# Performance work log

Hardware: AMD Instinct MI355X
Metric: run time of the kernel (lower is better)

The kernel has to match this reference:

```python
import jax, jax.numpy as jnp
import numpy as np
import math


def setup_inputs() -> dict:
    B, L, D, P, V = 4, 4096, 512, 128, 8
    key = jax.random.key(0)
    ki = iter(jax.random.split(key, 40))
    def rn(shape, s=0.02):
        return jax.random.normal(next(ki), shape, jnp.float32) * s
    z = lambda *s: jnp.zeros(s, jnp.float32)
    return dict(
        x=jax.random.normal(next(ki), (B, L, D), jnp.float32),
        W_omega=rn((D, D)), b_omega=z(D),
        omega_scale=jnp.full((D,), 0.01, jnp.float32),
        W_pi1=rn((D, D)), b_pi1=z(D), W_pi2=rn((D, D)), b_pi2=z(D),
        W_m1v=rn((D, D)), b_m1v=z(D),
        W_m1o=rn((D, D)), b_m1o=z(D),
        W_mag=rn((D, D)), b_mag=z(D),
        mag_scale=jnp.asarray(5.0, jnp.float32),
        W_qoff=rn((D, D)), b_qoff=z(D),
        W_kenc=rn((D, P)), b_kenc=z(P),
        W_venc=rn((D, V)), b_venc=z(V),
        W_sk1=rn((2 * D, D)), b_sk1=z(D),
        W_sk2=rn((D, P)), b_sk2=z(P),
        W_sg=rn((D, 1)), b_sg=z(1),
        W_kvo=rn((V, D)), b_kvo=z(D),
        ln_g=jnp.ones((4 * D,), jnp.float32), ln_b=z(4 * D),
        W_o1=rn((4 * D, 2 * D)), b_o1=z(2 * D),
        W_o2=rn((2 * D, D)), b_o2=z(D),
    )


def _lin(h, W, b):
    return h @ W + b


def _gelu(h):
    return jax.nn.gelu(h, approximate=False)  # torch nn.GELU default (erf)


def _forward(x, W_omega, b_omega, omega_scale, W_pi1, b_pi1, W_pi2, b_pi2,
             W_m1v, b_m1v, W_m1o, b_m1o, W_mag, b_mag, mag_scale,
             W_qoff, b_qoff, W_kenc, b_kenc, W_venc, b_venc,
             W_sk1, b_sk1, W_sk2, b_sk2, W_sg, b_sg, W_kvo, b_kvo,
             ln_g, ln_b, W_o1, b_o1, W_o2, b_o2):
    B, L, D = x.shape
    P = W_kenc.shape[1]
    # --- evolving phases ---
    omega_scaled = _lin(x, W_omega, b_omega) * jnp.abs(omega_scale)
    phi_init = _lin(_gelu(_lin(x, W_pi1, b_pi1)), W_pi2, b_pi2)
    phi = phi_init + jnp.cumsum(omega_scaled, axis=1)
    cos_phi, sin_phi = jnp.cos(phi), jnp.sin(phi)
    # --- memory 1: positional phasor memory ---
    v1 = _lin(x, W_m1v, b_m1v)
    magnitude = jax.nn.sigmoid(_lin(x, W_mag, b_mag)) * jnp.abs(mag_scale)
    wv1 = magnitude * v1
    sqrt_mag = jnp.sqrt(jnp.cumsum(magnitude, axis=1) + 1e-8)
    mem1_cos = jnp.cumsum(wv1 * cos_phi, axis=1) / sqrt_mag
    mem1_sin = jnp.cumsum(wv1 * sin_phi, axis=1) / sqrt_mag
    phi_q = phi + _lin(x, W_qoff, b_qoff)
    pos_ret = (mem1_cos * jnp.cos(phi_q) + mem1_sin * jnp.sin(phi_q)) / math.sqrt(D)
    pos_out = _lin(pos_ret, W_m1o, b_m1o)
    # --- memory 2: key/value phasor binding ---
    query_phase = jnp.tanh(_lin(x, W_kenc, b_kenc)) * math.pi
    values = _lin(x, W_venc, b_venc)                      # [B,L,V]
    store_gate = jax.nn.sigmoid(_lin(x, W_sg, b_sg))      # [B,L,1]
    positions = jnp.arange(1, L + 1, dtype=x.dtype)[None, :, None]
    context_avg = jnp.cumsum(x, axis=1) / positions
    sk_in = jnp.concatenate([x, context_avg], axis=-1)
    storage_phase = jnp.tanh(_lin(_gelu(_lin(sk_in, W_sk1, b_sk1)), W_sk2, b_sk2)) * math.pi
    store_cos, store_sin = jnp.cos(storage_phase), jnp.sin(storage_phase)  # [B,L,P]
    gv = values * store_gate                               # [B,L,V]
    # [B,L,P,V] outer products, cumsum along L
    kv_mem_cos = jnp.cumsum(store_cos[..., None] * gv[:, :, None, :], axis=1)
    kv_mem_sin = jnp.cumsum(store_sin[..., None] * gv[:, :, None, :], axis=1)
    gate_cum = jnp.clip(jnp.cumsum(store_gate, axis=1), 1.0, None)  # [B,L,1]
    inv_norm = (1.0 / jnp.sqrt(gate_cum))[..., None]
    kv_mem_cos = kv_mem_cos * inv_norm
    kv_mem_sin = kv_mem_sin * inv_norm
    q_cos, q_sin = jnp.cos(query_phase), jnp.sin(query_phase)
    kv_retrieved = (jnp.einsum('blp,blpv->blv', q_cos, kv_mem_cos)
                    + jnp.einsum('blp,blpv->blv', q_sin, kv_mem_sin)) / math.sqrt(P)
    kv_out = _lin(kv_retrieved, W_kvo, b_kvo)
    # --- output projection ---
    combined = jnp.concatenate([pos_out, kv_out, x * cos_phi, x * sin_phi], axis=-1)
    mu = combined.mean(axis=-1, keepdims=True)
    var = combined.var(axis=-1, keepdims=True)
    h = (combined - mu) / jnp.sqrt(var + 1e-5) * ln_g + ln_b
    h = _gelu(_lin(h, W_o1, b_o1))  # dropout is identity in eval mode
    return x + _lin(h, W_o2, b_o2)


def reference(x, W_omega, b_omega, omega_scale, W_pi1, b_pi1, W_pi2, b_pi2,
              W_m1v, b_m1v, W_m1o, b_m1o, W_mag, b_mag, mag_scale,
              W_qoff, b_qoff, W_kenc, b_kenc, W_venc, b_venc,
              W_sk1, b_sk1, W_sk2, b_sk2, W_sg, b_sg, W_kvo, b_kvo,
              ln_g, ln_b, W_o1, b_o1, W_o2, b_o2):
    return _forward(x, W_omega, b_omega, omega_scale, W_pi1, b_pi1, W_pi2, b_pi2,
                    W_m1v, b_m1v, W_m1o, b_m1o, W_mag, b_mag, mag_scale,
                    W_qoff, b_qoff, W_kenc, b_kenc, W_venc, b_venc,
                    W_sk1, b_sk1, W_sk2, b_sk2, W_sg, b_sg, W_kvo, b_kvo,
                    ln_g, ln_b, W_o1, b_o1, W_o2, b_o2)
```

## Files before the change

### kernel.cpp

```cpp
#include <hip/hip_runtime.h>
#include <math.h>

#define B_ 4
#define L_ 4096
#define D_ 512
#define P_ 128
#define V_ 8
#define N_ (B_*L_)
#define NC 64
#define CL (L_/NC)
#define LD ((size_t)L_*D_)
#define PI_F 3.14159265358979323846f

typedef unsigned short ushort;
typedef __attribute__((ext_vector_type(8))) short bh8;
typedef __attribute__((ext_vector_type(4))) float f4;
typedef const __attribute__((address_space(1))) unsigned int gu32;
typedef __attribute__((address_space(3))) unsigned int lu32;

__device__ __forceinline__ float geluf(float v){
    return 0.5f*v*(1.0f+erff(v*0.7071067811865475f));
}
__device__ __forceinline__ float tanhf_fast(float x){
    return 1.0f - 2.0f/(__expf(2.0f*x)+1.0f);
}
__device__ __forceinline__ ushort f2b(float f){
    union { float f; unsigned u; } v; v.f = f;
    unsigned r = (v.u + 0x7fffu + ((v.u >> 16) & 1u)) >> 16;
    return (ushort)r;
}
__device__ __forceinline__ float b2f(ushort h){
    union { unsigned u; float f; } v; v.u = ((unsigned)h) << 16;
    return v.f;
}
__device__ __forceinline__ void gload16(const ushort* g, ushort* l){
    __builtin_amdgcn_global_load_lds((gu32*)g, (lu32*)l, 16, 0, 0);
}
__device__ __forceinline__ int xcd_swz(int orig, int nwg){
    int q8 = nwg >> 3, r8 = nwg & 7;
    int xcd = orig & 7, sub = orig >> 3;
    return (xcd < r8 ? xcd*(q8+1) : r8*(q8+1) + (xcd-r8)*q8) + sub;
}

template<int ACT>
__global__ __launch_bounds__(512, 1)
void egemm_k(const ushort* __restrict__ A, int lda,
             const ushort* __restrict__ Wt, const float* __restrict__ bias,
             ushort* __restrict__ Ob, float* __restrict__ Of,
             int ldc, int K, const float* __restrict__ addbuf)
{
    __shared__ ushort lA[2][256*64];
    __shared__ ushort lB[2][256*64];
    const int tid = threadIdx.x, lane = tid & 63, w = tid >> 6;
    const int wr = w >> 2, wc = w & 3;
    const int nbx = gridDim.x;
    const int wg = xcd_swz(blockIdx.y*nbx + blockIdx.x, nbx*gridDim.y);
    const int row0 = (wg / nbx) * 256, col0 = (wg % nbx) * 256;

    f4 zero4 = {0.f,0.f,0.f,0.f};
    f4 acc[8][4];
    #pragma unroll
    for (int i=0;i<8;i++)
        #pragma unroll
        for (int j=0;j<4;j++) acc[i][j] = zero4;

    auto stage = [&](int buf, int kt){
        #pragma unroll
        for (int is=0; is<4; ++is){
            int id = tid + is*512;
            int r = id >> 3, p = id & 7;
            int srcc = (p ^ (r & 7)) * 8;
            gload16(A + (size_t)(row0 + r)*lda + kt + srcc, &lA[buf][r*64 + p*8]);
        }
        #pragma unroll
        for (int is=0; is<4; ++is){
            int id = tid + is*512;
            int r = id >> 3, p = id & 7;
            int srcc = (p ^ (r & 7)) * 8;
            gload16(Wt + (size_t)(col0 + r)*K + kt + srcc, &lB[buf][r*64 + p*8]);
        }
    };

    const int NT = K >> 6;
    stage(0, 0);
    for (int t2 = 0; t2 < NT; ++t2){
        int cur = t2 & 1;
        if (t2 + 1 < NT){
            stage(cur ^ 1, (t2+1) << 6);
            asm volatile("s_waitcnt vmcnt(8)" ::: "memory");
        } else {
            asm volatile("s_waitcnt vmcnt(0)" ::: "memory");
        }
        __builtin_amdgcn_s_barrier();
        __builtin_amdgcn_sched_barrier(0);
        __builtin_amdgcn_s_setprio(1);
        #pragma unroll
        for (int h=0; h<2; ++h){
            bh8 af[8], bf_[4];
            #pragma unroll
            for (int i=0;i<8;i++){
                int row = wr*128 + i*16 + (lane & 15);
                int pc = (h*4 + (lane >> 4)) ^ (row & 7);
                af[i] = *(const bh8*)&lA[cur][row*64 + pc*8];
            }
            #pragma unroll
            for (int j=0;j<4;j++){
                int row = wc*64 + j*16 + (lane & 15);
                int pc = (h*4 + (lane >> 4)) ^ (row & 7);
                bf_[j] = *(const bh8*)&lB[cur][row*64 + pc*8];
            }
            #pragma unroll
            for (int i=0;i<8;i++)
                #pragma unroll
                for (int j=0;j<4;j++)
                    acc[i][j] = __builtin_amdgcn_mfma_f32_16x16x32_bf16(af[i], bf_[j], acc[i][j], 0, 0, 0);
        }
        __builtin_amdgcn_s_setprio(0);
        __builtin_amdgcn_sched_barrier(0);
        __builtin_amdgcn_s_barrier();
    }

    #pragma unroll
    for (int i=0;i<8;i++){
        int rr = row0 + wr*128 + i*16 + ((lane >> 4) << 2);
        #pragma unroll
        for (int j=0;j<4;j++){
            int cc = col0 + wc*64 + j*16 + (lane & 15);
            float bv = bias[cc];
            #pragma unroll
            for (int q=0;q<4;q++){
                int r = rr + q;
                float t = acc[i][j][q] + bv;
                if (ACT==2){
                    if (addbuf) t += addbuf[(size_t)r*512 + cc];
                    Of[(size_t)r*ldc + cc] = t;
                } else {
                    if (ACT==1) t = geluf(t);
                    Ob[(size_t)r*ldc + cc] = f2b(t);
                }
            }
        }
    }
}

__global__ __launch_bounds__(256, 2)
void fgemm_k(const ushort* __restrict__ A, int lda, const ushort* __restrict__ Wt,
             const float* __restrict__ bs0, const float* __restrict__ bs1,
             const float* __restrict__ bs2, const float* __restrict__ bs3,
             const float* __restrict__ bs4, const float* __restrict__ bs5,
             ushort* __restrict__ o0, ushort* __restrict__ o1p, ushort* __restrict__ o2p,
             ushort* __restrict__ o3p, ushort* __restrict__ o4p,
             ushort* __restrict__ Qc, ushort* __restrict__ Qs,
             const float* __restrict__ omsc, const float* __restrict__ magscp, int K)
{
    __shared__ ushort lA[2][128*32];
    __shared__ ushort lB[2][128*32];
    const int tid = threadIdx.x, lane = tid & 63, w = tid >> 6;
    const int wr = w >> 1, wc = w & 1;
    const int nbx = gridDim.x;
    const int wg = xcd_swz(blockIdx.y*nbx + blockIdx.x, nbx*gridDim.y);
    const int row0 = (wg / nbx) * 128, col0 = (wg % nbx) * 128;

    const int srow = w*32 + (lane >> 2);
    const int scol = (lane & 3) * 8;
    const ushort* gA0 = A  + (size_t)(row0 + srow)      * lda + scol;
    const ushort* gA1 = A  + (size_t)(row0 + srow + 16) * lda + scol;
    const ushort* gB0 = Wt + (size_t)(col0 + srow)      * K   + scol;
    const ushort* gB1 = Wt + (size_t)(col0 + srow + 16) * K   + scol;
    const int d0 = srow*32 + scol, d1 = (srow+16)*32 + scol;

    f4 zero4 = {0.f,0.f,0.f,0.f};
    f4 acc[4][4];
    #pragma unroll
    for (int i=0;i<4;i++)
        #pragma unroll
        for (int j=0;j<4;j++) acc[i][j] = zero4;

    const int fr = lane & 15, fq = (lane >> 4) * 8;
    gload16(gA0, &lA[0][d0]); gload16(gA1, &lA[0][d1]);
    gload16(gB0, &lB[0][d0]); gload16(gB1, &lB[0][d1]);
    __syncthreads();
    int cur = 0;
    for (int kt = 0; kt < K; kt += 32) {
        int nxt = cur ^ 1;
        if (kt + 32 < K) {
            gload16(gA0 + kt + 32, &lA[nxt][d0]); gload16(gA1 + kt + 32, &lA[nxt][d1]);
            gload16(gB0 + kt + 32, &lB[nxt][d0]); gload16(gB1 + kt + 32, &lB[nxt][d1]);
        }
        bh8 af[4], bfr[4];
        #pragma unroll
        for (int i=0;i<4;i++){
            af[i]  = *(const bh8*)&lA[cur][(wr*64 + i*16 + fr)*32 + fq];
            bfr[i] = *(const bh8*)&lB[cur][(wc*64 + i*16 + fr)*32 + fq];
        }
        #pragma unroll
        for (int i=0;i<4;i++)
            #pragma unroll
            for (int j=0;j<4;j++)
                acc[i][j] = __builtin_amdgcn_mfma_f32_16x16x32_bf16(af[i], bfr[j], acc[i][j], 0, 0, 0);
        __syncthreads();
        cur = nxt;
    }

    const int seg = col0 >> 9;
    if (seg == 5) {
        #pragma unroll
        for (int i=0;i<4;i++){
            int rr = row0 + wr*64 + i*16 + ((lane >> 4) << 2);
            #pragma unroll
            for (int j=0;j<4;j++){
                int lcc = (col0 - 2560) + wc*64 + j*16 + (lane & 15);
                float bv = bs5[lcc];
                #pragma unroll
                for (int q=0;q<4;q++){
                    int r = rr + q;
                    float ph = tanhf_fast(acc[i][j][q] + bv)*PI_F;
                    Qc[(size_t)r*128 + lcc] = f2b(__cosf(ph));
                    Qs[(size_t)r*128 + lcc] = f2b(__sinf(ph));
                }
            }
        }
        return;
    }
    const float* bias = seg==0?bs0: seg==1?bs1: seg==2?bs2: seg==3?bs3: bs4;
    ushort* dst = seg==0?o0: seg==1?o1p: seg==2?o2p: seg==3?o3p: o4p;
    float msc = fabsf(*magscp);
    #pragma unroll
    for (int i=0;i<4;i++){
        int rr = row0 + wr*64 + i*16 + ((lane >> 4) << 2);
        #pragma unroll
        for (int j=0;j<4;j++){
            int cc = col0 + wc*64 + j*16 + (lane & 15);
            int lcc = cc & 511;
            float bv = bias[lcc];
            float csc = (seg==0) ? fabsf(omsc[lcc]) : 1.0f;
            #pragma unroll
            for (int q=0;q<4;q++){
                int r = rr + q;
                float t = acc[i][j][q] + bv;
                if (seg==1)      t = msc/(1.0f+__expf(-t));
                else if (seg==3) t = geluf(t);
                else             t *= csc;
                dst[(size_t)r*512 + lcc] = f2b(t);
            }
        }
    }
}

__global__ __launch_bounds__(256, 2)
void mgemm_k(const ushort* __restrict__ Apos, const ushort* __restrict__ Ask,
             const ushort* __restrict__ Wm1o, const ushort* __restrict__ Wsk2,
             const float* __restrict__ bm1o, const float* __restrict__ bsk2,
             ushort* __restrict__ planes, ushort* __restrict__ Kc, ushort* __restrict__ Ks)
{
    __shared__ ushort lA[2][128*32];
    __shared__ ushort lB[2][128*32];
    const int tid = threadIdx.x, lane = tid & 63, w = tid >> 6;
    const int wr = w >> 1, wc = w & 1;
    const int nbx = gridDim.x;
    const int wg = xcd_swz(blockIdx.y*nbx + blockIdx.x, nbx*gridDim.y);
    const int row0 = (wg / nbx) * 128, col0 = (wg % nbx) * 128;
    const int seg = col0 >> 9;
    const ushort* A  = seg ? Ask  : Apos;
    const ushort* Wt = seg ? Wsk2 : Wm1o;
    const int wcol0 = seg ? (col0 - 512) : col0;
    const int K = 512;

    const int srow = w*32 + (lane >> 2);
    const int scol = (lane & 3) * 8;
    const ushort* gA0 = A  + (size_t)(row0 + srow)       * 512 + scol;
    const ushort* gA1 = A  + (size_t)(row0 + srow + 16)  * 512 + scol;
    const ushort* gB0 = Wt + (size_t)(wcol0 + srow)      * 512 + scol;
    const ushort* gB1 = Wt + (size_t)(wcol0 + srow + 16) * 512 + scol;
    const int d0 = srow*32 + scol, d1 = (srow+16)*32 + scol;

    f4 zero4 = {0.f,0.f,0.f,0.f};
    f4 acc[4][4];
    #pragma unroll
    for (int i=0;i<4;i++)
        #pragma unroll
        for (int j=0;j<4;j++) acc[i][j] = zero4;

    const int fr = lane & 15, fq = (lane >> 4) * 8;
    gload16(gA0, &lA[0][d0]); gload16(gA1, &lA[0][d1]);
    gload16(gB0, &lB[0][d0]); gload16(gB1, &lB[0][d1]);
    __syncthreads();
    int cur = 0;
    for (int kt = 0; kt < K; kt += 32) {
        int nxt = cur ^ 1;
        if (kt + 32 < K) {
            gload16(gA0 + kt + 32, &lA[nxt][d0]); gload16(gA1 + kt + 32, &lA[nxt][d1]);
            gload16(gB0 + kt + 32, &lB[nxt][d0]); gload16(gB1 + kt + 32, &lB[nxt][d1]);
        }
        bh8 af[4], bfr[4];
        #pragma unroll
        for (int i=0;i<4;i++){
            af[i]  = *(const bh8*)&lA[cur][(wr*64 + i*16 + fr)*32 + fq];
            bfr[i] = *(const bh8*)&lB[cur][(wc*64 + i*16 + fr)*32 + fq];
        }
        #pragma unroll
        for (int i=0;i<4;i++)
            #pragma unroll
            for (int j=0;j<4;j++)
                acc[i][j] = __builtin_amdgcn_mfma_f32_16x16x32_bf16(af[i], bfr[j], acc[i][j], 0, 0, 0);
        __syncthreads();
        cur = nxt;
    }

    #pragma unroll
    for (int i=0;i<4;i++){
        int rr = row0 + wr*64 + i*16 + ((lane >> 4) << 2);
        #pragma unroll
        for (int j=0;j<4;j++){
            int cc = col0 + wc*64 + j*16 + (lane & 15);
            #pragma unroll
            for (int q=0;q<4;q++){
                int r = rr + q;
                if (seg == 0){
                    planes[(size_t)r*2048 + cc] = f2b(acc[i][j][q] + bm1o[cc]);
                } else {
                    int lcc = cc - 512;
                    float ph = tanhf_fast(acc[i][j][q] + bsk2[lcc])*PI_F;
                    Kc[(size_t)r*128 + lcc] = f2b(__cosf(ph));
                    Ks[(size_t)r*128 + lcc] = f2b(__sinf(ph));
                }
            }
        }
    }
}

struct WtArgs {
    const float* src[12];
    ushort* dst[12];
    int K[12], M[12], t0[13];
};
__global__ __launch_bounds__(256)
void wtall_k(WtArgs a)
{
    __shared__ float tile[32][33];
    int bb = blockIdx.x;
    int j = 0;
    while (bb >= a.t0[j+1]) ++j;
    int tt = bb - a.t0[j];
    int K = a.K[j], M = a.M[j];
    int mt = M >> 5;
    int kb = (tt / mt) * 32, mb = (tt % mt) * 32;
    const float* W = a.src[j]; ushort* Wt = a.dst[j];
    int tx = threadIdx.x & 31, ty = threadIdx.x >> 5;
    #pragma unroll
    for (int i = ty; i < 32; i += 8)
        tile[i][tx] = W[(size_t)(kb+i)*M + mb+tx];
    __syncthreads();
    #pragma unroll
    for (int i = ty; i < 32; i += 8)
        Wt[(size_t)(mb+i)*K + kb+tx] = f2b(tile[tx][i]);
}

__global__ __launch_bounds__(256)
void fconv_k(const float* __restrict__ in, ushort* __restrict__ xctx)
{
    size_t i = ((size_t)blockIdx.x*256 + threadIdx.x) * 4;
    size_t row = i >> 9; int d = (int)(i & 511);
    float4 v = *(const float4*)(in + i);
    ushort* o = xctx + row*1024 + d;
    o[0]=f2b(v.x); o[1]=f2b(v.y); o[2]=f2b(v.z); o[3]=f2b(v.w);
}

__global__ __launch_bounds__(256)
void s1a_k(const ushort* __restrict__ omega, const float* __restrict__ xg,
           float* __restrict__ csA, float* __restrict__ csX)
{
    int bid = blockIdx.x;
    int b = bid >> 7; int rem = bid & 127;
    int dg = rem & 1, c = rem >> 1;
    int d = dg*256 + threadIdx.x;
    size_t base = ((size_t)b*L_ + (size_t)c*CL)*D_ + d;
    float sA=0.f, sX=0.f;
    for (int l=0;l<CL;l++){
        sA += b2f(omega[base + (size_t)l*D_]);
        sX += xg[base + (size_t)l*D_];
    }
    size_t ci = ((size_t)b*NC + c)*D_ + d;
    csA[ci]=sA; csX[ci]=sX;
}

__global__ __launch_bounds__(256)
void aux1_k(float* __restrict__ csA, float* __restrict__ csX,
            const float* __restrict__ sgate, float* __restrict__ rinv, int nb2)
{
    __shared__ float wsum[4];
    __shared__ float carry;
    int bb = blockIdx.x, t = threadIdx.x;
    if (bb < nb2){
        int tt = bb*256 + t;
        int b = tt >> 9, d = tt & 511;
        float* bufs[2] = {csA, csX};
        #pragma unroll
        for (int i=0;i<2;i++){
            float* p = bufs[i] + ((size_t)b*NC)*D_ + d;
            float run=0.f;
            for (int c=0;c<NC;c++){
                float v = p[(size_t)c*D_];
                p[(size_t)c*D_] = run;
                run += v;
            }
        }
        return;
    }
    int b = bb - nb2;
    int lane = t & 63, wave = t >> 6;
    if (t == 0) carry = 0.f;
    __syncthreads();
    for (int s = 0; s < L_/256; s++){
        float v = sgate[(size_t)b*L_ + s*256 + t];
        float sc = v;
        #pragma unroll
        for (int off=1; off<64; off<<=1){
            float u = __shfl_up(sc, off, 64);
            if (lane >= off) sc += u;
        }
        if (lane == 63) wsum[wave] = sc;
        __syncthreads();
        float woff = carry;
        for (int w2 = 0; w2 < wave; w2++) woff += wsum[w2];
        float inc = sc + woff;
        rinv[(size_t)b*L_ + s*256 + t] = rsqrtf(fmaxf(inc, 1.0f));
        __syncthreads();
        if (t == 255) carry = inc;
        __syncthreads();
    }
}

__global__ void prefix_k(float* a, float* b2v, float* c3, int nbuf)
{
    int t = blockIdx.x*blockDim.x + threadIdx.x;
    int b = t >> 9, d = t & 511;
    float* bufs[3] = {a,b2v,c3};
    for (int i=0;i<nbuf;i++){
        float* p = bufs[i] + ((size_t)b*NC)*D_ + d;
        float run=0.f;
        for (int c=0;c<NC;c++){
            float v = p[(size_t)c*D_];
            p[(size_t)c*D_] = run;
            run += v;
        }
    }
}

__global__ __launch_bounds__(256)
void s1c_k(const ushort* __restrict__ omega, const float* __restrict__ xg,
           const ushort* __restrict__ phi_init,
           const ushort* __restrict__ magn, const ushort* __restrict__ v1,
           const float* __restrict__ csA, const float* __restrict__ csX,
           ushort* __restrict__ cphi, ushort* __restrict__ sphi, ushort* __restrict__ xctx,
           float* __restrict__ csM, float* __restrict__ csC, float* __restrict__ csS)
{
    int bid = blockIdx.x;
    int b = bid >> 7; int rem = bid & 127;
    int dg = rem & 1, c = rem >> 1;
    int d = dg*256 + threadIdx.x;
    size_t ci = ((size_t)b*NC + c)*D_ + d;
    float phiacc = csA[ci], xacc = csX[ci];
    float sM=0.f,sC=0.f,sS=0.f;
    size_t xrow = (size_t)b*L_ + (size_t)c*CL;
    size_t base = xrow*D_ + d;
    for (int l=0;l<CL;l++){
        size_t idx = base + (size_t)l*D_;
        phiacc += b2f(omega[idx]);
        float ph = b2f(phi_init[idx]) + phiacc;
        float spv = __sinf(ph), cpv = __cosf(ph);
        cphi[idx] = f2b(cpv); sphi[idx] = f2b(spv);
        xacc += xg[idx];
        xctx[(xrow + l)*1024 + 512 + d] = f2b(__fdividef(xacc, (float)(c*CL + l + 1)));
        float m = b2f(magn[idx]); sM += m;
        float wv = m * b2f(v1[idx]);
        sC = fmaf(wv, cpv, sC); sS = fmaf(wv, spv, sS);
    }
    csM[ci]=sM; csC[ci]=sC; csS[ci]=sS;
}

__global__ __launch_bounds__(256)
void s1e_k(const ushort* __restrict__ magn, const ushort* __restrict__ v1,
           const ushort* qoff, const ushort* __restrict__ cphi, const ushort* __restrict__ sphi,
           const float* __restrict__ csM, const float* __restrict__ csC,
           const float* __restrict__ csS, ushort* pos_ret)
{
    int bid = blockIdx.x;
    int b = bid >> 7; int rem = bid & 127;
    int dg = rem & 1, c = rem >> 1;
    int d = dg*256 + threadIdx.x;
    size_t ci = ((size_t)b*NC + c)*D_ + d;
    float mA=csM[ci], cA=csC[ci], sA=csS[ci];
    size_t base = ((size_t)b*L_ + (size_t)c*CL)*D_ + d;
    for (int l=0;l<CL;l++){
        size_t idx = base + (size_t)l*D_;
        float m = b2f(magn[idx]); mA += m;
        float wv = m * b2f(v1[idx]);
        float cp = b2f(cphi[idx]), sp = b2f(sphi[idx]);
        cA = fmaf(wv, cp, cA); sA = fmaf(wv, sp, sA);
        float rs = rsqrtf(mA + 1e-8f);
        float qo = b2f(qoff[idx]);
        float sq = __sinf(qo), cq = __cosf(qo);
        float cosq = cp*cq - sp*sq;
        float sinq = sp*cq + cp*sq;
        pos_ret[idx] = f2b((cA*cosq + sA*sinq) * rs * 0.04419417382415922f);
    }
}

__global__ __launch_bounds__(256)
void vencsg_k(const float* __restrict__ xg, const float* __restrict__ Wv,
              const float* __restrict__ bv, const float* __restrict__ Wg,
              const float* __restrict__ bg,
              ushort* __restrict__ gvb, float* __restrict__ sgate)
{
    int gw = (int)((blockIdx.x*(size_t)blockDim.x + threadIdx.x) >> 6);
    int lane = threadIdx.x & 63;
    const float* xr = xg + (size_t)gw*D_;
    float pv[8] = {0,0,0,0,0,0,0,0}; float pg = 0.f;
    #pragma unroll
    for (int j=0;j<8;j++){
        int k = lane + 64*j;
        float xv = xr[k];
        #pragma unroll
        for (int v=0;v<8;v++) pv[v] = fmaf(xv, Wv[k*8+v], pv[v]);
        pg = fmaf(xv, Wg[k], pg);
    }
    #pragma unroll
    for (int off=32; off>0; off>>=1){
        #pragma unroll
        for (int v=0;v<8;v++) pv[v] += __shfl_down(pv[v], off, 64);
        pg += __shfl_down(pg, off, 64);
    }
    if (lane==0){
        float sg = 1.0f/(1.0f+__expf(-(pg + bg[0])));
        #pragma unroll
        for (int v=0;v<8;v++) gvb[(size_t)gw*8+v] = f2b((pv[v] + bv[v]) * sg);
        sgate[gw] = sg;
    }
}

__global__ __launch_bounds__(256)
void kvsum_k(const ushort* __restrict__ Kc, const ushort* __restrict__ Ks,
             const ushort* __restrict__ gvb, float* __restrict__ csKV)
{
    int bid = blockIdx.x;
    int b = bid >> 6, c = bid & 63;
    int t = threadIdx.x; int p = t & 127; int v0 = (t>>7)*4;
    size_t row0 = (size_t)b*L_ + (size_t)c*64;
    float ac[4]={0,0,0,0}, as[4]={0,0,0,0};
    for (int l=0;l<64;l++){
        size_t r = row0 + l;
        float kc = b2f(Kc[r*(size_t)P_ + p]);
        float ks = b2f(Ks[r*(size_t)P_ + p]);
        #pragma unroll
        for (int j=0;j<4;j++){
            float gv = b2f(gvb[r*(size_t)V_ + v0 + j]);
            ac[j] = fmaf(kc, gv, ac[j]);
            as[j] = fmaf(ks, gv, as[j]);
        }
    }
    float* base = csKV + ((size_t)b*64 + c)*2048;
    #pragma unroll
    for (int j=0;j<4;j++){
        base[p*V_ + v0 + j] = ac[j];
        base[1024 + p*V_ + v0 + j] = as[j];
    }
}

__global__ void kvpfx_k(float* __restrict__ csKV)
{
    int t = blockIdx.x*blockDim.x + threadIdx.x;
    int b = t >> 11, si = t & 2047;
    float* ptr = csKV + ((size_t)b*64)*2048 + si;
    float run=0.f;
    for (int c=0;c<64;c++){
        float v = ptr[(size_t)c*2048];
        ptr[(size_t)c*2048] = run;
        run += v;
    }
}

__global__ __launch_bounds__(256)
void kv2_k(const ushort* __restrict__ Qc, const ushort* __restrict__ Qs,
           const ushort* __restrict__ Kc, const ushort* __restrict__ Ks,
           const ushort* __restrict__ gvb, const float* __restrict__ rinv,
           const float* __restrict__ csKV, float* __restrict__ kvret)
{
    __shared__ ushort sS[64][66];
    __shared__ float sM[2048];
    __shared__ float sgv[64][8];
    int tile = blockIdx.x, b = blockIdx.y;
    int t = threadIdx.x, lane = t & 63, w = t >> 6;
    int wr = w >> 1, wc = w & 1;
    size_t row0 = (size_t)b*L_ + (size_t)tile*64;
    const float* kvb = csKV + ((size_t)b*64 + tile)*2048;
    #pragma unroll
    for (int k=0;k<8;k++) sM[t + k*256] = kvb[t + k*256];
    #pragma unroll
    for (int k=0;k<2;k++){
        int idx = t + k*256; int l = idx >> 3, v = idx & 7;
        sgv[l][v] = b2f(gvb[(row0 + l)*(size_t)V_ + v]);
    }
    f4 zero4 = {0.f,0.f,0.f,0.f};
    f4 acc[2][2];
    #pragma unroll
    for (int i=0;i<2;i++)
        #pragma unroll
        for (int j=0;j<2;j++) acc[i][j] = zero4;
    #pragma unroll
    for (int ks=0; ks<8; ks++){
        const ushort* Ab = (ks<4) ? Qc : Qs;
        const ushort* Bb = (ks<4) ? Kc : Ks;
        int kb = (ks&3)*32 + (lane>>4)*8;
        bh8 af[2], bfr[2];
        #pragma unroll
        for (int i=0;i<2;i++)
            af[i] = *(const bh8*)(Ab + (row0 + wr*32 + i*16 + (lane&15))*(size_t)P_ + kb);
        #pragma unroll
        for (int j=0;j<2;j++)
            bfr[j] = *(const bh8*)(Bb + (row0 + wc*32 + j*16 + (lane&15))*(size_t)P_ + kb);
        #pragma unroll
        for (int i=0;i<2;i++)
            #pragma unroll
            for (int j=0;j<2;j++)
                acc[i][j] = __builtin_amdgcn_mfma_f32_16x16x32_bf16(af[i], bfr[j], acc[i][j], 0, 0, 0);
    }
    #pragma unroll
    for (int i=0;i<2;i++){
        #pragma unroll
        for (int j=0;j<2;j++){
            int cc = wc*32 + j*16 + (lane & 15);
            #pragma unroll
            for (int q=0;q<4;q++){
                int lr = wr*32 + i*16 + ((lane>>4)<<2) + q;
                sS[lr][cc] = f2b((cc <= lr) ? acc[i][j][q] : 0.f);
            }
        }
    }
    __syncthreads();
    int l = t & 63, vh = t >> 6; int v0 = vh*2;
    const ushort* qcr = Qc + (row0 + l)*(size_t)P_;
    const ushort* qsr = Qs + (row0 + l)*(size_t)P_;
    float a0=0.f, a1=0.f;
    #pragma unroll
    for (int pc=0; pc<16; pc++){
        bh8 qc8 = *(const bh8*)(qcr + pc*8);
        bh8 qs8 = *(const bh8*)(qsr + pc*8);
        #pragma unroll
        for (int e=0;e<8;e++){
            int p = pc*8+e;
            float qc = b2f((ushort)qc8[e]), qs = b2f((ushort)qs8[e]);
            a0 += qc*sM[p*8+v0]   + qs*sM[1024+p*8+v0];
            a1 += qc*sM[p*8+v0+1] + qs*sM[1024+p*8+v0+1];
        }
    }
    for (int c=0;c<64;c++){
        float sv = b2f(sS[l][c]);
        a0 = fmaf(sv, sgv[c][v0],   a0);
        a1 = fmaf(sv, sgv[c][v0+1], a1);
    }
    float rn = rinv[row0 + l] * 0.08838834764831845f;
    kvret[(row0+l)*(size_t)V_ + v0]   = a0*rn;
    kvret[(row0+l)*(size_t)V_ + v0+1] = a1*rn;
}

__global__ __launch_bounds__(256)
void cmb_k(const float* __restrict__ xg, const ushort* __restrict__ cphi,
           const ushort* __restrict__ sphi,
           const float* __restrict__ kvret, const float* __restrict__ Wkvo,
           const float* __restrict__ bkvo,
           const float* __restrict__ ln_g, const float* __restrict__ ln_b,
           ushort* pl)
{
    __shared__ float red[8];
    __shared__ float kvv[8];
    int n = blockIdx.x; int t = threadIdx.x;
    int wave = t>>6, lane = t&63;
    if (t < 8) kvv[t] = kvret[(size_t)n*8 + t];
    __syncthreads();
    float v_[8]; float sum=0.f, sumsq=0.f;
    #pragma unroll
    for (int i=0;i<8;i++){
        int cidx = t + i*256;
        int seg = cidx >> 9, cc = cidx & 511;
        float v;
        if (seg == 0) v = b2f(pl[(size_t)n*2048 + cidx]);
        else if (seg == 1) {
            v = bkvo[cc];
            #pragma unroll
            for (int vv=0; vv<8; vv++) v = fmaf(kvv[vv], Wkvo[vv*512 + cc], v);
        } else {
            size_t id = (size_t)n*D_ + cc;
            v = xg[id] * b2f((seg==2) ? cphi[id] : sphi[id]);
        }
        v_[i]=v; sum += v; sumsq = fmaf(v,v,sumsq);
    }
    #pragma unroll
    for (int off=32; off>0; off>>=1){
        sum += __shfl_xor(sum, off, 64);
        sumsq += __shfl_xor(sumsq, off, 64);
    }
    if (lane==0){ red[wave]=sum; red[wave+4]=sumsq; }
    __syncthreads();
    float s = red[0]+red[1]+red[2]+red[3];
    float q = red[4]+red[5]+red[6]+red[7];
    float mu = s * (1.0f/2048.0f);
    float var = q * (1.0f/2048.0f) - mu*mu;
    float rstd = rsqrtf(var + 1e-5f);
    #pragma unroll
    for (int i=0;i<8;i++){
        int cidx = t + i*256;
        float h = (v_[i]-mu)*rstd*ln_g[cidx] + ln_b[cidx];
        pl[(size_t)n*2048 + cidx] = f2b(h);
    }
}

__global__ void copyx_k(const float* __restrict__ x, float* __restrict__ out, size_t n)
{
    size_t i = (size_t)blockIdx.x*256 + threadIdx.x;
    if (i < n) out[i] = x[i];
}

struct WS {
    ushort *wt_fused,*wt_pi2,*wt_sk1,*wt_sk2,*wt_m1o,*wt_o1,*wt_o2;
    ushort *xctx, *pool;
    ushort *Qc,*Qs,*Kc,*Ks,*gvb,*cphi,*sphi;
    float *sgate,*rinv,*kvret;
    float *csA,*csX,*csM,*csC,*csS,*csKV;
};

static size_t ws_layout(WS& w, char* base, int NB)
{
    size_t off = 0;
    auto al = [&](size_t bytes)->char* {
        char* p = base + off; off = (off + bytes + 255) & ~(size_t)255; return p;
    };
    size_t R = (size_t)NB * L_;
    w.wt_fused=(ushort*)al((size_t)2688*512*2);
    w.wt_pi2 =(ushort*)al(512*512*2);
    w.wt_sk1 =(ushort*)al((size_t)512*1024*2); w.wt_sk2=(ushort*)al(128*512*2);
    w.wt_m1o =(ushort*)al(512*512*2);
    w.wt_o1  =(ushort*)al((size_t)1024*2048*2); w.wt_o2=(ushort*)al((size_t)512*1024*2);
    w.xctx=(ushort*)al(R*1024*2);
    w.pool=(ushort*)al(R*512*2*6);
    w.Qc=(ushort*)al(R*128*2); w.Qs=(ushort*)al(R*128*2);
    w.Kc=(ushort*)al(R*128*2); w.Ks=(ushort*)al(R*128*2);
    w.gvb=(ushort*)al(R*8*2);
    w.cphi=(ushort*)al(R*512*2); w.sphi=(ushort*)al(R*512*2);
    w.sgate=(float*)al(R*4); w.rinv=(float*)al(R*4); w.kvret=(float*)al(R*8*4);
    w.csA=(float*)al((size_t)NB*NC*512*4); w.csX=(float*)al((size_t)NB*NC*512*4);
    w.csM=(float*)al((size_t)NB*NC*512*4); w.csC=(float*)al((size_t)NB*NC*512*4);
    w.csS=(float*)al((size_t)NB*NC*512*4);
    w.csKV=(float*)al((size_t)NB*64*2048*4);
    return off;
}

extern "C" void kernel_launch(void* const* d_in, const int* in_sizes, int n_in,
                              void* d_out, int out_size, void* d_ws, size_t ws_size,
                              hipStream_t stream)
{
    const float* x        =(const float*)d_in[0];
    const float* W_omega  =(const float*)d_in[1];  const float* b_omega=(const float*)d_in[2];
    const float* omega_sc =(const float*)d_in[3];
    const float* W_pi1    =(const float*)d_in[4];  const float* b_pi1 =(const float*)d_in[5];
    const float* W_pi2    =(const float*)d_in[6];  const float* b_pi2 =(const float*)d_in[7];
    const float* W_m1v    =(const float*)d_in[8];  const float* b_m1v =(const float*)d_in[9];
    const float* W_m1o    =(const float*)d_in[10]; const float* b_m1o =(const float*)d_in[11];
    const float* W_mag    =(const float*)d_in[12]; const float* b_mag =(const float*)d_in[13];
    const float* mag_sc   =(const float*)d_in[14];
    const float* W_qoff   =(const float*)d_in[15]; const float* b_qoff=(const float*)d_in[16];
    const float* W_kenc   =(const float*)d_in[17]; const float* b_kenc=(const float*)d_in[18];
    const float* W_venc   =(const float*)d_in[19]; const float* b_venc=(const float*)d_in[20];
    const float* W_sk1    =(const float*)d_in[21]; const float* b_sk1 =(const float*)d_in[22];
    const float* W_sk2    =(const float*)d_in[23]; const float* b_sk2 =(const float*)d_in[24];
    const float* W_sg     =(const float*)d_in[25]; const float* b_sg  =(const float*)d_in[26];
    const float* W_kvo    =(const float*)d_in[27]; const float* b_kvo =(const float*)d_in[28];
    const float* ln_g     =(const float*)d_in[29]; const float* ln_b  =(const float*)d_in[30];
    const float* W_o1     =(const float*)d_in[31]; const float* b_o1  =(const float*)d_in[32];
    const float* W_o2     =(const float*)d_in[33]; const float* b_o2  =(const float*)d_in[34];
    float* out = (float*)d_out;

    char* wsb = (char*)d_ws;
    WS w;
    int NB = 4;
    if (ws_layout(w, wsb, 4) > ws_size) {
        NB = 2;
        if (ws_layout(w, wsb, 2) > ws_size) {
            NB = 1;
            if (ws_layout(w, wsb, 1) > ws_size) {
                copyx_k<<<dim3((unsigned)(((size_t)N_*D_ + 255)/256)), dim3(256), 0, stream>>>(x, out, (size_t)N_*D_);
                return;
            }
        }
    }

    dim3 blk(256);
    WtArgs wa;
    const float* srcs[12] = {W_omega, W_mag, W_m1v, W_pi1, W_qoff, W_kenc,
                             W_pi2, W_sk1, W_sk2, W_m1o, W_o1, W_o2};
    ushort* dsts[12] = {w.wt_fused + (size_t)0*512*512, w.wt_fused + (size_t)1*512*512,
                        w.wt_fused + (size_t)2*512*512, w.wt_fused + (size_t)3*512*512,
                        w.wt_fused + (size_t)4*512*512, w.wt_fused + (size_t)5*512*512,
                        w.wt_pi2, w.wt_sk1, w.wt_sk2, w.wt_m1o, w.wt_o1, w.wt_o2};
    int Ks_[12] = {512,512,512,512,512,512, 512,1024,512,512,2048,1024};
    int Ms_[12] = {512,512,512,512,512,128, 512, 512,128,512,1024, 512};
    int cum = 0;
    for (int j = 0; j < 12; ++j){
        wa.src[j]=srcs[j]; wa.dst[j]=dsts[j]; wa.K[j]=Ks_[j]; wa.M[j]=Ms_[j];
        wa.t0[j]=cum; cum += (Ks_[j]/32)*(Ms_[j]/32);
    }
    wa.t0[12]=cum;
    wtall_k<<<dim3(cum), blk, 0, stream>>>(wa);

    const int R = NB * L_;
    const size_t SL = (size_t)R * 512;
    ushort* bA = w.pool;        ushort* bB = w.pool + SL;
    ushort* bC = w.pool + 2*SL; ushort* bD = w.pool + 3*SL;
    ushort* bE = w.pool + 4*SL; ushort* bF = w.pool + 5*SL;
    ushort* planes = w.pool;
    ushort* h1 = w.pool + 4*SL;

    #define EGEMM(ACT,A,lda,Wt_,bias_,Ob_,Of_,ldc,K_,M_,add_) \
        egemm_k<ACT><<<dim3((M_)/256, R/256), dim3(512), 0, stream>>>(A,lda,Wt_,bias_,Ob_,Of_,ldc,K_,add_)

    for (int g = 0; g < B_/NB; ++g) {
        const float* xg = x + (size_t)g*NB*LD;
        float* outg = out + (size_t)g*NB*LD;

        fconv_k<<<dim3((unsigned)((size_t)R*512/1024)), blk, 0, stream>>>(xg, w.xctx);

        fgemm_k<<<dim3(2688/128, R/128), blk, 0, stream>>>(
            w.xctx,1024, w.wt_fused, b_omega,b_mag,b_m1v,b_pi1,b_qoff,b_kenc,
            bA,bB,bC,bD,bF, w.Qc,w.Qs, omega_sc, mag_sc, 512);
        EGEMM(0, bD,512, w.wt_pi2, b_pi2, bE,(float*)0, 512, 512,512, (const float*)0);
        vencsg_k<<<dim3((unsigned)((size_t)R*64/256)), blk, 0, stream>>>(xg, W_venc,b_venc, W_sg,b_sg, w.gvb, w.sgate);
        s1a_k<<<dim3(NB*NC*2), blk, 0, stream>>>(bA, xg, w.csA, w.csX);
        aux1_k<<<dim3(NB*2 + NB), blk, 0, stream>>>(w.csA, w.csX, w.sgate, w.rinv, NB*2);
        s1c_k<<<dim3(NB*NC*2), blk, 0, stream>>>(bA, xg, bE, bB, bC, w.csA, w.csX,
                                                 w.cphi, w.sphi, w.xctx, w.csM, w.csC, w.csS);
        prefix_k<<<dim3(NB*2), blk, 0, stream>>>(w.csM, w.csC, w.csS, 3);
        s1e_k<<<dim3(NB*NC*2), blk, 0, stream>>>(bB, bC, bF, w.cphi, w.sphi,
                                                 w.csM, w.csC, w.csS, bF);

        EGEMM(1, w.xctx,1024, w.wt_sk1, b_sk1, bE,(float*)0, 512, 1024,512, (const float*)0);
        mgemm_k<<<dim3(640/128, R/128), blk, 0, stream>>>(
            bF, bE, w.wt_m1o, w.wt_sk2, b_m1o, b_sk2, planes, w.Kc, w.Ks);

        kvsum_k<<<dim3(NB*64), blk, 0, stream>>>(w.Kc, w.Ks, w.gvb, w.csKV);
        kvpfx_k<<<dim3(NB*8), blk, 0, stream>>>(w.csKV);
        kv2_k<<<dim3(64, NB), blk, 0, stream>>>(w.Qc, w.Qs, w.Kc, w.Ks, w.gvb, w.rinv, w.csKV, w.kvret);

        cmb_k<<<dim3(R), blk, 0, stream>>>(xg, w.cphi, w.sphi, w.kvret, W_kvo, b_kvo,
                                           ln_g, ln_b, planes);
        EGEMM(1, planes,2048, w.wt_o1, b_o1, h1,(float*)0, 1024, 2048,1024, (const float*)0);
        EGEMM(2, h1,1024, w.wt_o2, b_o2, (ushort*)0,outg, 512, 1024,512, xg);
    }
    #undef EGEMM
}
```

Baseline: 528.2 us.

## Use 128x128 BK64 swizzled GEMM loop for narrow GEMMs and fused kernels

Adds a shared 128x128-tile K-loop macro with 64-wide K steps, XOR-swizzled LDS staging and vmcnt-based double buffering. The fused-input and memory-output GEMM kernels now use it in place of their 32-wide K loops. A new dgemm_k with 256 threads and two blocks per CU uses the same loop and replaces the 256x256 egemm for the 512-column GEMMs (pi2, sk1, o2). The aim is more workgroups on the narrow GEMMs and fewer barriers per K step, paid for with more LDS per block and smaller tiles that reuse less data.

New measurement: 500.8 us. -5.2%, faster.

```diff
diff --git a/kernel.cpp b/kernel.cpp
--- a/kernel.cpp
+++ b/kernel.cpp
@@ -42,87 +42,90 @@
     return (xcd < r8 ? xcd*(q8+1) : r8*(q8+1) + (xcd-r8)*q8) + sub;
 }
 
+#define KLOOP_128(A_, lda_, Wt_, wK_, accv)                                     \
+    {                                                                           \
+        auto stage = [&](int buf, int kt){                                      \
+            _Pragma("unroll")                                                   \
+            for (int is=0; is<4; ++is){                                         \
+                int id = tid + is*256;                                          \
+                int r = id >> 3, p = id & 7;                                    \
+                int srcc = (p ^ (r & 7)) * 8;                                   \
+                gload16(A_ + (size_t)(row0 + r)*lda_ + kt + srcc, &lA[buf][r*64 + p*8]); \
+            }                                                                   \
+            _Pragma("unroll")                                                   \
+            for (int is=0; is<4; ++is){                                         \
+                int id = tid + is*256;                                          \
+                int r = id >> 3, p = id & 7;                                    \
+                int srcc = (p ^ (r & 7)) * 8;                                   \
+                gload16(Wt_ + (size_t)(wcol0 + r)*wK_ + kt + srcc, &lB[buf][r*64 + p*8]); \
+            }                                                                   \
+        };                                                                      \
+        const int NT = wK_ >> 6;                                                \
+        stage(0, 0);                                                            \
+        for (int t2 = 0; t2 < NT; ++t2){                                        \
+            int cur = t2 & 1;                                                   \
+            if (t2 + 1 < NT){                                                   \
+                stage(cur ^ 1, (t2+1) << 6);                                    \
+                asm volatile("s_waitcnt vmcnt(8)" ::: "memory");                \
+            } else {                                                            \
+                asm volatile("s_waitcnt vmcnt(0)" ::: "memory");                \
+            }                                                                   \
+            __builtin_amdgcn_s_barrier();                                       \
+            __builtin_amdgcn_sched_barrier(0);                                  \
+            _Pragma("unroll")                                                   \
+            for (int h=0; h<2; ++h){                                            \
+                bh8 af[4], bf_[4];                                              \
+                _Pragma("unroll")                                               \
+                for (int i=0;i<4;i++){                                          \
+                    int row = wr*64 + i*16 + (lane & 15);                       \
+                    int pc = (h*4 + (lane >> 4)) ^ (row & 7);                   \
+                    af[i] = *(const bh8*)&lA[cur][row*64 + pc*8];               \
+                }                                                               \
+                _Pragma("unroll")                                               \
+                for (int j=0;j<4;j++){                                          \
+                    int row = wc*64 + j*16 + (lane & 15);                       \
+                    int pc = (h*4 + (lane >> 4)) ^ (row & 7);                   \
+                    bf_[j] = *(const bh8*)&lB[cur][row*64 + pc*8];              \
+                }                                                               \
+                _Pragma("unroll")                                               \
+                for (int i=0;i<4;i++)                                           \
+                    _Pragma("unroll")                                           \
+                    for (int j=0;j<4;j++)                                       \
+                        accv[i][j] = __builtin_amdgcn_mfma_f32_16x16x32_bf16(af[i], bf_[j], accv[i][j], 0, 0, 0); \
+            }                                                                   \
+            __builtin_amdgcn_sched_barrier(0);                                  \
+            __builtin_amdgcn_s_barrier();                                       \
+        }                                                                       \
+    }
+
 template<int ACT>
-__global__ __launch_bounds__(512, 1)
-void egemm_k(const ushort* __restrict__ A, int lda,
+__global__ __launch_bounds__(256, 2)
+void dgemm_k(const ushort* __restrict__ A, int lda,
              const ushort* __restrict__ Wt, const float* __restrict__ bias,
              ushort* __restrict__ Ob, float* __restrict__ Of,
              int ldc, int K, const float* __restrict__ addbuf)
 {
-    __shared__ ushort lA[2][256*64];
-    __shared__ ushort lB[2][256*64];
+    __shared__ ushort lA[2][128*64];
+    __shared__ ushort lB[2][128*64];
     const int tid = threadIdx.x, lane = tid & 63, w = tid >> 6;
-    const int wr = w >> 2, wc = w & 3;
+    const int wr = w >> 1, wc = w & 1;
     const int nbx = gridDim.x;
     const int wg = xcd_swz(blockIdx.y*nbx + blockIdx.x, nbx*gridDim.y);
-    const int row0 = (wg / nbx) * 256, col0 = (wg % nbx) * 256;
+    const int row0 = (wg / nbx) * 128, col0 = (wg % nbx) * 128;
+    const int wcol0 = col0;
 
     f4 zero4 = {0.f,0.f,0.f,0.f};
-    f4 acc[8][4];
-    #pragma unroll
-    for (int i=0;i<8;i++)
+    f4 acc[4][4];
+    #pragma unroll
+    for (int i=0;i<4;i++)
         #pragma unroll
         for (int j=0;j<4;j++) acc[i][j] = zero4;
 
-    auto stage = [&](int buf, int kt){
-        #pragma unroll
-        for (int is=0; is<4; ++is){
-            int id = tid + is*512;
-            int r = id >> 3, p = id & 7;
-            int srcc = (p ^ (r & 7)) * 8;
-            gload16(A + (size_t)(row0 + r)*lda + kt + srcc, &lA[buf][r*64 + p*8]);
-        }
-        #pragma unroll
-        for (int is=0; is<4; ++is){
-            int id = tid + is*512;
-            int r = id >> 3, p = id & 7;
-            int srcc = (p ^ (r & 7)) * 8;
-            gload16(Wt + (size_t)(col0 + r)*K + kt + srcc, &lB[buf][r*64 + p*8]);
-        }
-    };
-
-    const int NT = K >> 6;
-    stage(0, 0);
-    for (int t2 = 0; t2 < NT; ++t2){
-        int cur = t2 & 1;
-        if (t2 + 1 < NT){
-            stage(cur ^ 1, (t2+1) << 6);
-            asm volatile("s_waitcnt vmcnt(8)" ::: "memory");
-        } else {
-            asm volatile("s_waitcnt vmcnt(0)" ::: "memory");
-        }
-        __builtin_amdgcn_s_barrier();
-        __builtin_amdgcn_sched_barrier(0);
-        __builtin_amdgcn_s_setprio(1);
-        #pragma unroll
-        for (int h=0; h<2; ++h){
-            bh8 af[8], bf_[4];
-            #pragma unroll
-            for (int i=0;i<8;i++){
-                int row = wr*128 + i*16 + (lane & 15);
-                int pc = (h*4 + (lane >> 4)) ^ (row & 7);
-                af[i] = *(const bh8*)&lA[cur][row*64 + pc*8];
-            }
-            #pragma unroll
-            for (int j=0;j<4;j++){
-                int row = wc*64 + j*16 + (lane & 15);
-                int pc = (h*4 + (lane >> 4)) ^ (row & 7);
-                bf_[j] = *(const bh8*)&lB[cur][row*64 + pc*8];
-            }
-            #pragma unroll
-            for (int i=0;i<8;i++)
-                #pragma unroll
-                for (int j=0;j<4;j++)
-                    acc[i][j] = __builtin_amdgcn_mfma_f32_16x16x32_bf16(af[i], bf_[j], acc[i][j], 0, 0, 0);
-        }
-        __builtin_amdgcn_s_setprio(0);
-        __builtin_amdgcn_sched_barrier(0);
-        __builtin_amdgcn_s_barrier();
-    }
-
-    #pragma unroll
-    for (int i=0;i<8;i++){
-        int rr = row0 + wr*128 + i*16 + ((lane >> 4) << 2);
+    KLOOP_128(A, lda, Wt, K, acc)
+
+    #pragma unroll
+    for (int i=0;i<4;i++){
+        int rr = row0 + wr*64 + i*16 + ((lane >> 4) << 2);
         #pragma unroll
         for (int j=0;j<4;j++){
             int cc = col0 + wc*64 + j*16 + (lane & 15);
@@ -143,6 +146,107 @@
     }
 }
 
+template<int ACT>
+__global__ __launch_bounds__(512, 1)
+void egemm_k(const ushort* __restrict__ A, int lda,
+             const ushort* __restrict__ Wt, const float* __restrict__ bias,
+             ushort* __restrict__ Ob, float* __restrict__ Of,
+             int ldc, int K, const float* __restrict__ addbuf)
+{
+    __shared__ ushort lA[2][256*64];
+    __shared__ ushort lB[2][256*64];
+    const int tid = threadIdx.x, lane = tid & 63, w = tid >> 6;
+    const int wr = w >> 2, wc = w & 3;
+    const int nbx = gridDim.x;
+    const int wg = xcd_swz(blockIdx.y*nbx + blockIdx.x, nbx*gridDim.y);
+    const int row0 = (wg / nbx) * 256, col0 = (wg % nbx) * 256;
+
+    f4 zero4 = {0.f,0.f,0.f,0.f};
+    f4 acc[8][4];
+    #pragma unroll
+    for (int i=0;i<8;i++)
+        #pragma unroll
+        for (int j=0;j<4;j++) acc[i][j] = zero4;
+
+    auto stage = [&](int buf, int kt){
+        #pragma unroll
+        for (int is=0; is<4; ++is){
+            int id = tid + is*512;
+            int r = id >> 3, p = id & 7;
+            int srcc = (p ^ (r & 7)) * 8;
+            gload16(A + (size_t)(row0 + r)*lda + kt + srcc, &lA[buf][r*64 + p*8]);
+        }
+        #pragma unroll
+        for (int is=0; is<4; ++is){
+            int id = tid + is*512;
+            int r = id >> 3, p = id & 7;
+            int srcc = (p ^ (r & 7)) * 8;
+            gload16(Wt + (size_t)(col0 + r)*K + kt + srcc, &lB[buf][r*64 + p*8]);
+        }
+    };
+
+    const int NT = K >> 6;
+    stage(0, 0);
+    for (int t2 = 0; t2 < NT; ++t2){
+        int cur = t2 & 1;
+        if (t2 + 1 < NT){
+            stage(cur ^ 1, (t2+1) << 6);
+            asm volatile("s_waitcnt vmcnt(8)" ::: "memory");
+        } else {
+            asm volatile("s_waitcnt vmcnt(0)" ::: "memory");
+        }
+        __builtin_amdgcn_s_barrier();
+        __builtin_amdgcn_sched_barrier(0);
+        __builtin_amdgcn_s_setprio(1);
+        #pragma unroll
+        for (int h=0; h<2; ++h){
+            bh8 af[8], bf_[4];
+            #pragma unroll
+            for (int i=0;i<8;i++){
+                int row = wr*128 + i*16 + (lane & 15);
+                int pc = (h*4 + (lane >> 4)) ^ (row & 7);
+                af[i] = *(const bh8*)&lA[cur][row*64 + pc*8];
+            }
+            #pragma unroll
+            for (int j=0;j<4;j++){
+                int row = wc*64 + j*16 + (lane & 15);
+                int pc = (h*4 + (lane >> 4)) ^ (row & 7);
+                bf_[j] = *(const bh8*)&lB[cur][row*64 + pc*8];
+            }
+            #pragma unroll
+            for (int i=0;i<8;i++)
+                #pragma unroll
+                for (int j=0;j<4;j++)
+                    acc[i][j] = __builtin_amdgcn_mfma_f32_16x16x32_bf16(af[i], bf_[j], acc[i][j], 0, 0, 0);
+        }
+        __builtin_amdgcn_s_setprio(0);
+        __builtin_amdgcn_sched_barrier(0);
+        __builtin_amdgcn_s_barrier();
+    }
+
+    #pragma unroll
+    for (int i=0;i<8;i++){
+        int rr = row0 + wr*128 + i*16 + ((lane >> 4) << 2);
+        #pragma unroll
+        for (int j=0;j<4;j++){
+            int cc = col0 + wc*64 + j*16 + (lane & 15);
+            float bv = bias[cc];
+            #pragma unroll
+            for (int q=0;q<4;q++){
+                int r = rr + q;
+                float t = acc[i][j][q] + bv;
+                if (ACT==2){
+                    if (addbuf) t += addbuf[(size_t)r*512 + cc];
+                    Of[(size_t)r*ldc + cc] = t;
+                } else {
+                    if (ACT==1) t = geluf(t);
+                    Ob[(size_t)r*ldc + cc] = f2b(t);
+                }
+            }
+        }
+    }
+}
+
 __global__ __launch_bounds__(256, 2)
 void fgemm_k(const ushort* __restrict__ A, int lda, const ushort* __restrict__ Wt,
              const float* __restrict__ bs0, const float* __restrict__ bs1,
@@ -153,21 +257,14 @@
              ushort* __restrict__ Qc, ushort* __restrict__ Qs,
              const float* __restrict__ omsc, const float* __restrict__ magscp, int K)
 {
-    __shared__ ushort lA[2][128*32];
-    __shared__ ushort lB[2][128*32];
+    __shared__ ushort lA[2][128*64];
+    __shared__ ushort lB[2][128*64];
     const int tid = threadIdx.x, lane = tid & 63, w = tid >> 6;
     const int wr = w >> 1, wc = w & 1;
     const int nbx = gridDim.x;
     const int wg = xcd_swz(blockIdx.y*nbx + blockIdx.x, nbx*gridDim.y);
     const int row0 = (wg / nbx) * 128, col0 = (wg % nbx) * 128;
-
-    const int srow = w*32 + (lane >> 2);
-    const int scol = (lane & 3) * 8;
-    const ushort* gA0 = A  + (size_t)(row0 + srow)      * lda + scol;
-    const ushort* gA1 = A  + (size_t)(row0 + srow + 16) * lda + scol;
-    const ushort* gB0 = Wt + (size_t)(col0 + srow)      * K   + scol;
-    const ushort* gB1 = Wt + (size_t)(col0 + srow + 16) * K   + scol;
-    const int d0 = srow*32 + scol, d1 = (srow+16)*32 + scol;
+    const int wcol0 = col0;
 
     f4 zero4 = {0.f,0.f,0.f,0.f};
     f4 acc[4][4];
@@ -176,31 +273,7 @@
         #pragma unroll
         for (int j=0;j<4;j++) acc[i][j] = zero4;
 
-    const int fr = lane & 15, fq = (lane >> 4) * 8;
-    gload16(gA0, &lA[0][d0]); gload16(gA1, &lA[0][d1]);
-    gload16(gB0, &lB[0][d0]); gload16(gB1, &lB[0][d1]);
-    __syncthreads();
-    int cur = 0;
-    for (int kt = 0; kt < K; kt += 32) {
-        int nxt = cur ^ 1;
-        if (kt + 32 < K) {
-            gload16(gA0 + kt + 32, &lA[nxt][d0]); gload16(gA1 + kt + 32, &lA[nxt][d1]);
-            gload16(gB0 + kt + 32, &lB[nxt][d0]); gload16(gB1 + kt + 32, &lB[nxt][d1]);
-        }
-        bh8 af[4], bfr[4];
-        #pragma unroll
-        for (int i=0;i<4;i++){
-            af[i]  = *(const bh8*)&lA[cur][(wr*64 + i*16 + fr)*32 + fq];
-            bfr[i] = *(const bh8*)&lB[cur][(wc*64 + i*16 + fr)*32 + fq];
-        }
-        #pragma unroll
-        for (int i=0;i<4;i++)
-            #pragma unroll
-            for (int j=0;j<4;j++)
-                acc[i][j] = __builtin_amdgcn_mfma_f32_16x16x32_bf16(af[i], bfr[j], acc[i][j], 0, 0, 0);
-        __syncthreads();
-        cur = nxt;
-    }
+    KLOOP_128(A, lda, Wt, K, acc)
 
     const int seg = col0 >> 9;
     if (seg == 5) {
@@ -253,8 +326,8 @@
              const float* __restrict__ bm1o, const float* __restrict__ bsk2,
              ushort* __restrict__ planes, ushort* __restrict__ Kc, ushort* __restrict__ Ks)
 {
-    __shared__ ushort lA[2][128*32];
-    __shared__ ushort lB[2][128*32];
+    __shared__ ushort lA[2][128*64];
+    __shared__ ushort lB[2][128*64];
     const int tid = threadIdx.x, lane = tid & 63, w = tid >> 6;
     const int wr = w >> 1, wc = w & 1;
     const int nbx = gridDim.x;
@@ -264,15 +337,7 @@
     const ushort* A  = seg ? Ask  : Apos;
     const ushort* Wt = seg ? Wsk2 : Wm1o;
     const int wcol0 = seg ? (col0 - 512) : col0;
-    const int K = 512;
-
-    const int srow = w*32 + (lane >> 2);
-    const int scol = (lane & 3) * 8;
-    const ushort* gA0 = A  + (size_t)(row0 + srow)       * 512 + scol;
-    const ushort* gA1 = A  + (size_t)(row0 + srow + 16)  * 512 + scol;
-    const ushort* gB0 = Wt + (size_t)(wcol0 + srow)      * 512 + scol;
-    const ushort* gB1 = Wt + (size_t)(wcol0 + srow + 16) * 512 + scol;
-    const int d0 = srow*32 + scol, d1 = (srow+16)*32 + scol;
+    const int K = 512, lda = 512;
 
     f4 zero4 = {0.f,0.f,0.f,0.f};
     f4 acc[4][4];
@@ -281,31 +346,7 @@
         #pragma unroll
         for (int j=0;j<4;j++) acc[i][j] = zero4;
 
-    const int fr = lane & 15, fq = (lane >> 4) * 8;
-    gload16(gA0, &lA[0][d0]); gload16(gA1, &lA[0][d1]);
-    gload16(gB0, &lB[0][d0]); gload16(gB1, &lB[0][d1]);
-    __syncthreads();
-    int cur = 0;
-    for (int kt = 0; kt < K; kt += 32) {
-        int nxt = cur ^ 1;
-        if (kt + 32 < K) {
-            gload16(gA0 + kt + 32, &lA[nxt][d0]); gload16(gA1 + kt + 32, &lA[nxt][d1]);
-            gload16(gB0 + kt + 32, &lB[nxt][d0]); gload16(gB1 + kt + 32, &lB[nxt][d1]);
-        }
-        bh8 af[4], bfr[4];
-        #pragma unroll
-        for (int i=0;i<4;i++){
-            af[i]  = *(const bh8*)&lA[cur][(wr*64 + i*16 + fr)*32 + fq];
-            bfr[i] = *(const bh8*)&lB[cur][(wc*64 + i*16 + fr)*32 + fq];
-        }
-        #pragma unroll
-        for (int i=0;i<4;i++)
-            #pragma unroll
-            for (int j=0;j<4;j++)
-                acc[i][j] = __builtin_amdgcn_mfma_f32_16x16x32_bf16(af[i], bfr[j], acc[i][j], 0, 0, 0);
-        __syncthreads();
-        cur = nxt;
-    }
+    KLOOP_128(A, lda, Wt, K, acc)
 
     #pragma unroll
     for (int i=0;i<4;i++){
@@ -820,6 +861,8 @@
     ushort* planes = w.pool;
     ushort* h1 = w.pool + 4*SL;
 
+    #define DGEMM(ACT,A,lda,Wt_,bias_,Ob_,Of_,ldc,K_,M_,add_) \
+        dgemm_k<ACT><<<dim3((M_)/128, R/128), blk, 0, stream>>>(A,lda,Wt_,bias_,Ob_,Of_,ldc,K_,add_)
     #define EGEMM(ACT,A,lda,Wt_,bias_,Ob_,Of_,ldc,K_,M_,add_) \
         egemm_k<ACT><<<dim3((M_)/256, R/256), dim3(512), 0, stream>>>(A,lda,Wt_,bias_,Ob_,Of_,ldc,K_,add_)
 
@@ -832,7 +875,7 @@
         fgemm_k<<<dim3(2688/128, R/128), blk, 0, stream>>>(
             w.xctx,1024, w.wt_fused, b_omega,b_mag,b_m1v,b_pi1,b_qoff,b_kenc,
             bA,bB,bC,bD,bF, w.Qc,w.Qs, omega_sc, mag_sc, 512);
-        EGEMM(0, bD,512, w.wt_pi2, b_pi2, bE,(float*)0, 512, 512,512, (const float*)0);
+        DGEMM(0, bD,512, w.wt_pi2, b_pi2, bE,(float*)0, 512, 512,512, (const float*)0);
         vencsg_k<<<dim3((unsigned)((size_t)R*64/256)), blk, 0, stream>>>(xg, W_venc,b_venc, W_sg,b_sg, w.gvb, w.sgate);
         s1a_k<<<dim3(NB*NC*2), blk, 0, stream>>>(bA, xg, w.csA, w.csX);
         aux1_k<<<dim3(NB*2 + NB), blk, 0, stream>>>(w.csA, w.csX, w.sgate, w.rinv, NB*2);
@@ -842,7 +885,7 @@
         s1e_k<<<dim3(NB*NC*2), blk, 0, stream>>>(bB, bC, bF, w.cphi, w.sphi,
                                                  w.csM, w.csC, w.csS, bF);
 
-        EGEMM(1, w.xctx,1024, w.wt_sk1, b_sk1, bE,(float*)0, 512, 1024,512, (const float*)0);
+        DGEMM(1, w.xctx,1024, w.wt_sk1, b_sk1, bE,(float*)0, 512, 1024,512, (const float*)0);
         mgemm_k<<<dim3(640/128, R/128), blk, 0, stream>>>(
             bF, bE, w.wt_m1o, w.wt_sk2, b_m1o, b_sk2, planes, w.Kc, w.Ks);
 
@@ -853,7 +896,8 @@
         cmb_k<<<dim3(R), blk, 0, stream>>>(xg, w.cphi, w.sphi, w.kvret, W_kvo, b_kvo,
                                            ln_g, ln_b, planes);
         EGEMM(1, planes,2048, w.wt_o1, b_o1, h1,(float*)0, 1024, 2048,1024, (const float*)0);
-        EGEMM(2, h1,1024, w.wt_o2, b_o2, (ushort*)0,outg, 512, 1024,512, xg);
-    }
+        DGEMM(2, h1,1024, w.wt_o2, b_o2, (ushort*)0,outg, 512, 1024,512, xg);
+    }
+    #undef DGEMM
     #undef EGEMM
 }
```
